# Optimization experiments

Hardware: AMD Instinct MI355X
Metric: run time of the kernel (lower is better)

The kernel has to match this reference:

```python
import jax, jax.numpy as jnp
import numpy as np

FEAT = 1024
SUPPORT = 512
N = 4096


def setup_inputs() -> dict:
    key = jax.random.key(0)
    k1, k2, k3, k4, k5, k6 = jax.random.split(key, 6)
    s = 1.0 / np.sqrt(FEAT)
    f = jax.random.normal(k1, (N, FEAT), dtype=jnp.float32)
    G = jax.random.normal(k2, (SUPPORT, FEAT), dtype=jnp.float32)
    # PyTorch LSTMCell params: weight_ih [4*hidden, input], weight_hh [4*hidden, hidden]
    W_ih = jax.random.uniform(k3, (4 * FEAT, 2 * FEAT), minval=-s, maxval=s, dtype=jnp.float32)
    W_hh = jax.random.uniform(k4, (4 * FEAT, FEAT), minval=-s, maxval=s, dtype=jnp.float32)
    b_ih = jax.random.uniform(k5, (4 * FEAT,), minval=-s, maxval=s, dtype=jnp.float32)
    b_hh = jax.random.uniform(k6, (4 * FEAT,), minval=-s, maxval=s, dtype=jnp.float32)
    return {"f": f, "G": G, "W_ih": W_ih, "W_hh": W_hh, "b_ih": b_ih, "b_hh": b_hh, "n_ways": 20}


def _lstm_cell(x, h, c, W_ih, W_hh, b_ih, b_hh):
    # gates ordered i, f, g, o as in torch.nn.LSTMCell
    gates = x @ W_ih.T + b_ih + h @ W_hh.T + b_hh  # [N, 4*FEAT]
    i, fg, g, o = jnp.split(gates, 4, axis=1)
    i = jax.nn.sigmoid(i)
    fg = jax.nn.sigmoid(fg)
    g = jnp.tanh(g)
    o = jax.nn.sigmoid(o)
    c_new = fg * c + i * g
    h_new = o * jnp.tanh(c_new)
    return h_new, c_new


def reference(f, G, W_ih, W_hh, b_ih, b_hh, n_ways):
    h = f
    c = jnp.zeros_like(f)  # c_0 expanded, zeros (non-learned Variable)
    for _ in range(n_ways):
        logit_a = h @ G.T                      # [N, M]
        a = jax.nn.softmax(logit_a, axis=0)    # softmax over dim 0, as in original
        r = a @ G                              # [N, FEAT]
        x = jnp.concatenate((f, r), axis=1)    # [N, 2*FEAT]
        h, c = _lstm_cell(x, h, c, W_ih, W_hh, b_ih, b_hh)
        h = h + f
    return h
```

## Files before the change

### kernel.cpp

```cpp
#include <hip/hip_runtime.h>
#include <math.h>

#define NB    4096
#define FEAT  1024
#define MSUP  512
#define G4    4096
#define NWAYS 20

typedef _Float16 f16;
typedef f16 f16x8 __attribute__((ext_vector_type(8)));
typedef f16 f16x4 __attribute__((ext_vector_type(4)));
typedef float f32x4 __attribute__((ext_vector_type(4)));
typedef unsigned int u32;
#define GLOBAL_AS __attribute__((address_space(1)))
#define LDS_AS    __attribute__((address_space(3)))

__device__ __forceinline__ void load_lds16(const void* g, void* l) {
    __builtin_amdgcn_global_load_lds((const GLOBAL_AS u32*)g, (LDS_AS u32*)l, 16, 0, 0);
}

__device__ __forceinline__ float sigm(float x) { return 1.f / (1.f + __expf(-x)); }

template<int BM, int BN, int WROWS, int WCOLS, bool OUTF16, bool HASBIAS>
__global__ __launch_bounds__(256) void mfma_nt(
    void* __restrict__ Cv, int ldc,
    const f16* __restrict__ A1, int lda1, const f16* __restrict__ B1, int ldb1, int K1,
    const f16* __restrict__ A2, int lda2, const f16* __restrict__ B2, int ldb2, int K2,
    const f16* __restrict__ A3, int lda3, const f16* __restrict__ B3, int ldb3, int K3,
    const float* __restrict__ bias)
{
    constexpr int BK = 32;
    constexpr int WM = BM / WROWS, WN = BN / WCOLS;
    constexpr int FM = WM / 16,   FN = WN / 16;
    __shared__ f16 As[BM][BK];
    __shared__ f16 Bs[BN][BK];
    const int tid  = threadIdx.x;
    const int lane = tid & 63;
    const int wrow = (tid >> 6) % WROWS, wcol = (tid >> 6) / WROWS;
    const int bm = blockIdx.y * BM, bn = blockIdx.x * BN;
    const int lr = lane & 15, lq = lane >> 4;

    f32x4 acc[FM][FN] = {};

    #pragma unroll
    for (int pass = 0; pass < 3; ++pass) {
        const f16* A = pass == 0 ? A1 : (pass == 1 ? A2 : A3);
        const f16* B = pass == 0 ? B1 : (pass == 1 ? B2 : B3);
        const int lda = pass == 0 ? lda1 : (pass == 1 ? lda2 : lda3);
        const int ldb = pass == 0 ? ldb1 : (pass == 1 ? ldb2 : ldb3);
        const int K   = pass == 0 ? K1  : (pass == 1 ? K2  : K3);
        if (!A) break;
        #pragma unroll 1
        for (int k0 = 0; k0 < K; k0 += BK) {
            __syncthreads();
            #pragma unroll
            for (int t = 0; t < (BM * 4) / 256; ++t) {
                int c = t * 256 + tid;
                load_lds16(A + (size_t)(bm + (c >> 2)) * lda + k0 + (c & 3) * 8,
                           &As[0][0] + ((size_t)t * 256 + (tid & 192)) * 8);
            }
            #pragma unroll
            for (int t = 0; t < (BN * 4) / 256; ++t) {
                int c = t * 256 + tid;
                load_lds16(B + (size_t)(bn + (c >> 2)) * ldb + k0 + (c & 3) * 8,
                           &Bs[0][0] + ((size_t)t * 256 + (tid & 192)) * 8);
            }
            __syncthreads();
            f16x8 af[FM], bf[FN];
            #pragma unroll
            for (int i = 0; i < FM; ++i)
                af[i] = *(const f16x8*)&As[wrow * WM + i * 16 + lr][lq * 8];
            #pragma unroll
            for (int j = 0; j < FN; ++j)
                bf[j] = *(const f16x8*)&Bs[wcol * WN + j * 16 + lr][lq * 8];
            #pragma unroll
            for (int i = 0; i < FM; ++i)
                #pragma unroll
                for (int j = 0; j < FN; ++j)
                    acc[i][j] = __builtin_amdgcn_mfma_f32_16x16x32_f16(af[i], bf[j], acc[i][j], 0, 0, 0);
        }
    }

    #pragma unroll
    for (int i = 0; i < FM; ++i) {
        #pragma unroll
        for (int j = 0; j < FN; ++j) {
            const int col  = bn + wcol * WN + j * 16 + lr;
            const int row0 = bm + wrow * WM + i * 16 + lq * 4;
            float badd = HASBIAS ? bias[col] : 0.f;
            #pragma unroll
            for (int r = 0; r < 4; ++r) {
                size_t off = (size_t)(row0 + r) * ldc + col;
                float v = acc[i][j][r] + badd;
                if (OUTF16) ((f16*)Cv)[off] = (f16)v;
                else        ((float*)Cv)[off] = v;
            }
        }
    }
}

__global__ __launch_bounds__(256) void gates_fused(
    const f16* __restrict__ a,
    const f16* __restrict__ WrHi,
    const f16* __restrict__ WrLo,
    const f16* __restrict__ h,
    const f16* __restrict__ Whh,
    const f16* __restrict__ pre,
    const float* __restrict__ fin,
    float* __restrict__ cbuf,
    f16* __restrict__ hh,
    float* __restrict__ hout,
    int first, int writeH)
{
    constexpr int BM = 128, BN = 128, BK = 32;
    constexpr int WM = 64, WN = 64, FM = 4, FN = 4;
    __shared__ f16 As[BM][BK];
    __shared__ f16 BsH[BN][BK];
    __shared__ f16 BsL[BN][BK];
    const int tid  = threadIdx.x;
    const int lane = tid & 63;
    const int wrow = (tid >> 6) & 1, wcol = (tid >> 6) >> 1;
    const int bm = blockIdx.y * BM, bn = blockIdx.x * BN;
    const int lr = lane & 15, lq = lane >> 4;

    f32x4 acc[FM][FN] = {};

    #pragma unroll 1
    for (int k0 = 0; k0 < MSUP; k0 += BK) {
        __syncthreads();
        #pragma unroll
        for (int t = 0; t < 2; ++t) {
            int c = t * 256 + tid;
            load_lds16(a + (size_t)(bm + (c >> 2)) * MSUP + k0 + (c & 3) * 8,
                       &As[0][0] + ((size_t)t * 256 + (tid & 192)) * 8);
        }
        #pragma unroll
        for (int t = 0; t < 2; ++t) {
            int c = t * 256 + tid;
            load_lds16(WrHi + (size_t)(bn + (c >> 2)) * MSUP + k0 + (c & 3) * 8,
                       &BsH[0][0] + ((size_t)t * 256 + (tid & 192)) * 8);
        }
        #pragma unroll
        for (int t = 0; t < 2; ++t) {
            int c = t * 256 + tid;
            load_lds16(WrLo + (size_t)(bn + (c >> 2)) * MSUP + k0 + (c & 3) * 8,
                       &BsL[0][0] + ((size_t)t * 256 + (tid & 192)) * 8);
        }
        __syncthreads();
        f16x8 af[FM], bh[FN], bl[FN];
        #pragma unroll
        for (int i = 0; i < FM; ++i)
            af[i] = *(const f16x8*)&As[wrow * WM + i * 16 + lr][lq * 8];
        #pragma unroll
        for (int j = 0; j < FN; ++j) {
            bh[j] = *(const f16x8*)&BsH[wcol * WN + j * 16 + lr][lq * 8];
            bl[j] = *(const f16x8*)&BsL[wcol * WN + j * 16 + lr][lq * 8];
        }
        #pragma unroll
        for (int i = 0; i < FM; ++i)
            #pragma unroll
            for (int j = 0; j < FN; ++j) {
                acc[i][j] = __builtin_amdgcn_mfma_f32_16x16x32_f16(af[i], bh[j], acc[i][j], 0, 0, 0);
                acc[i][j] = __builtin_amdgcn_mfma_f32_16x16x32_f16(af[i], bl[j], acc[i][j], 0, 0, 0);
            }
    }

    #pragma unroll 1
    for (int k0 = 0; k0 < FEAT; k0 += BK) {
        __syncthreads();
        #pragma unroll
        for (int t = 0; t < 2; ++t) {
            int c = t * 256 + tid;
            load_lds16(h + (size_t)(bm + (c >> 2)) * FEAT + k0 + (c & 3) * 8,
                       &As[0][0] + ((size_t)t * 256 + (tid & 192)) * 8);
        }
        #pragma unroll
        for (int t = 0; t < 2; ++t) {
            int c = t * 256 + tid;
            load_lds16(Whh + (size_t)(bn + (c >> 2)) * FEAT + k0 + (c & 3) * 8,
                       &BsH[0][0] + ((size_t)t * 256 + (tid & 192)) * 8);
        }
        __syncthreads();
        f16x8 af[FM], bf[FN];
        #pragma unroll
        for (int i = 0; i < FM; ++i)
            af[i] = *(const f16x8*)&As[wrow * WM + i * 16 + lr][lq * 8];
        #pragma unroll
        for (int j = 0; j < FN; ++j)
            bf[j] = *(const f16x8*)&BsH[wcol * WN + j * 16 + lr][lq * 8];
        #pragma unroll
        for (int i = 0; i < FM; ++i)
            #pragma unroll
            for (int j = 0; j < FN; ++j)
                acc[i][j] = __builtin_amdgcn_mfma_f32_16x16x32_f16(af[i], bf[j], acc[i][j], 0, 0, 0);
    }

    const int q  = lane & 3;
    const int kk = (lane >> 2) & 3;
    #pragma unroll
    for (int i = 0; i < FM; ++i) {
        #pragma unroll
        for (int j = 0; j < FN; ++j) {
            const int cb   = bn + wcol * WN + j * 16;
            const int row0 = bm + wrow * WM + i * 16 + lq * 4;
            float x[4];
            #pragma unroll
            for (int r = 0; r < 4; ++r) x[r] = acc[i][j][r];
            float g4[4];
            #pragma unroll
            for (int k = 0; k < 4; ++k) {
                int srcq = (q + k) & 3;
                int src  = (lane & ~3) | srcq;
                g4[srcq] = __shfl(x[(q - k + 4) & 3], src, 64);
            }
            const int row  = row0 + q;
            const int feat = (cb >> 2) + kk;
            f16x4 p = *(const f16x4*)(pre + (size_t)row * G4 + cb + 4 * kk);
            const float i_ = sigm(g4[0] + (float)p[0]);
            const float f_ = sigm(g4[1] + (float)p[1]);
            const float g_ = tanhf(g4[2] + (float)p[2]);
            const float o_ = sigm(g4[3] + (float)p[3]);
            const size_t cid = ((size_t)(blockIdx.y * gridDim.x + blockIdx.x) * (FM * FN)
                                + i * FN + j) * 256 + tid;
            float cold = first ? 0.f : cbuf[cid];
            float cn = i_ * g_ + f_ * cold;
            cbuf[cid] = cn;
            float hn = o_ * tanhf(cn) + fin[(size_t)row * FEAT + feat];
            hh[(size_t)row * FEAT + feat] = (f16)hn;
            if (writeH) hout[(size_t)row * FEAT + feat] = hn;
        }
    }
}

__global__ __launch_bounds__(256) void softmax_rows_kernel(
    const float* __restrict__ X, f16* __restrict__ Y)
{
    const int row = blockIdx.x;
    const float* x = X + (size_t)row * NB;
    f16* y = Y + (size_t)row * NB;
    const int tid = threadIdx.x;
    float v[16];
    float mx = -1e30f;
    #pragma unroll
    for (int i = 0; i < 16; ++i) { v[i] = x[tid + (i << 8)]; mx = fmaxf(mx, v[i]); }
    #pragma unroll
    for (int off = 32; off > 0; off >>= 1) mx = fmaxf(mx, __shfl_down(mx, off));
    __shared__ float sm[4];
    if ((tid & 63) == 0) sm[tid >> 6] = mx;
    __syncthreads();
    mx = fmaxf(fmaxf(sm[0], sm[1]), fmaxf(sm[2], sm[3]));
    float s = 0.f;
    #pragma unroll
    for (int i = 0; i < 16; ++i) { v[i] = __expf(v[i] - mx); s += v[i]; }
    #pragma unroll
    for (int off = 32; off > 0; off >>= 1) s += __shfl_down(s, off);
    __shared__ float ss[4];
    if ((tid & 63) == 0) ss[tid >> 6] = s;
    __syncthreads();
    s = ss[0] + ss[1] + ss[2] + ss[3];
    const float inv = 1.f / s;
    #pragma unroll
    for (int i = 0; i < 16; ++i) y[tid + (i << 8)] = (f16)(v[i] * inv);
}

__global__ __launch_bounds__(256) void transpose_f16_kernel(
    const f16* __restrict__ in, f16* __restrict__ out, int R, int C)
{
    __shared__ f16 t[64][65];
    const int r0 = blockIdx.y * 64, c0 = blockIdx.x * 64;
    const int lr = threadIdx.x & 63, lw = threadIdx.x >> 6;
    #pragma unroll
    for (int i = 0; i < 16; ++i) {
        int rr = lw * 16 + i;
        t[rr][lr] = in[(size_t)(r0 + rr) * C + c0 + lr];
    }
    __syncthreads();
    #pragma unroll
    for (int i = 0; i < 16; ++i) {
        int cc = lw * 16 + i;
        out[(size_t)(c0 + cc) * R + r0 + lr] = t[lr][cc];
    }
}

__global__ __launch_bounds__(256) void cvt_f16_kernel(
    const float* __restrict__ in, f16* __restrict__ out, int n)
{
    int idx = (blockIdx.x * 256 + threadIdx.x) * 4;
    if (idx < n) {
        float4 v = *(const float4*)(in + idx);
        f16x4 o = {(f16)v.x, (f16)v.y, (f16)v.z, (f16)v.w};
        *(f16x4*)(out + idx) = o;
    }
}

__global__ __launch_bounds__(256) void cvt_perm_kernel(
    const float* __restrict__ in, f16* __restrict__ out, int ld)
{
    int idx = (blockIdx.x * 256 + threadIdx.x) * 4;
    int j = idx / ld, k = idx % ld;
    int dst = 4 * (j & 1023) + (j >> 10);
    float4 v = *(const float4*)(in + idx);
    f16x4 o = {(f16)v.x, (f16)v.y, (f16)v.z, (f16)v.w};
    *(f16x4*)(out + (size_t)dst * ld + k) = o;
}

__global__ __launch_bounds__(256) void bias_perm_kernel(
    const float* __restrict__ bih, const float* __restrict__ bhh, float* __restrict__ out)
{
    int j = blockIdx.x * 256 + threadIdx.x;
    out[4 * (j & 1023) + (j >> 10)] = bih[j] + bhh[j];
}

__global__ __launch_bounds__(256) void split_hilo_kernel(
    const float* __restrict__ in, f16* __restrict__ hi, f16* __restrict__ lo, int n)
{
    int idx = (blockIdx.x * 256 + threadIdx.x) * 4;
    if (idx < n) {
        float4 v = *(const float4*)(in + idx);
        f16x4 h = {(f16)v.x, (f16)v.y, (f16)v.z, (f16)v.w};
        f16x4 l = {(f16)(v.x - (float)h.x), (f16)(v.y - (float)h.y),
                   (f16)(v.z - (float)h.z), (f16)(v.w - (float)h.w)};
        *(f16x4*)(hi + idx) = h;
        *(f16x4*)(lo + idx) = l;
    }
}

extern "C" void kernel_launch(void* const* d_in, const int* in_sizes, int n_in,
                              void* d_out, int out_size, void* d_ws, size_t ws_size,
                              hipStream_t stream) {
    const float* f   = (const float*)d_in[0];
    const float* G   = (const float*)d_in[1];
    const float* Wih = (const float*)d_in[2];
    const float* Whh = (const float*)d_in[3];
    const float* bih = (const float*)d_in[4];
    const float* bhh = (const float*)d_in[5];
    float* h = (float*)d_out;

    char* W = (char*)d_ws;
    f16*   pre_h   = (f16*)(W);
    float* aT      = (float*)(W + (size_t)(32 << 20));
    f16*   aTh     = (f16*)(W + (size_t)(40 << 20));
    f16*   a_h     = (f16*)(W + (size_t)(44 << 20));
    float* cbuf    = (float*)(W + (size_t)(48 << 20));
    f16*   h0      = (f16*)(W + (size_t)(64 << 20));
    f16*   hA      = (f16*)(W + (size_t)(72 << 20));
    f16*   hB      = (f16*)(W + (size_t)(80 << 20));
    f16*   Wih_h   = (f16*)(W + (size_t)(88 << 20));
    f16*   Whh_h   = (f16*)(W + (size_t)(104 << 20));
    float* Wr32    = (float*)(W + (size_t)(112 << 20));
    f16*   Wr_hi   = (f16*)(W + (size_t)(120 << 20));
    f16*   Wr_lo   = (f16*)(W + (size_t)(124 << 20));
    f16*   G_h     = (f16*)(W + (size_t)(128 << 20));
    float* bias_p  = (float*)(W + (size_t)(129 << 20));

    const f16* NF = nullptr;
    const dim3 blk(256);

    cvt_f16_kernel<<<(NB * FEAT) / 1024, blk, 0, stream>>>(f, h0, NB * FEAT);
    cvt_perm_kernel<<<(G4 * 2 * FEAT) / 1024, blk, 0, stream>>>(Wih, Wih_h, 2 * FEAT);
    cvt_perm_kernel<<<(G4 * FEAT) / 1024, blk, 0, stream>>>(Whh, Whh_h, FEAT);
    cvt_f16_kernel<<<(MSUP * FEAT) / 1024, blk, 0, stream>>>(G, G_h, MSUP * FEAT);
    bias_perm_kernel<<<G4 / 256, blk, 0, stream>>>(bih, bhh, bias_p);

    mfma_nt<128, 128, 2, 2, true, true><<<dim3(G4 / 128, NB / 128), blk, 0, stream>>>(
        pre_h, G4,
        h0, FEAT, Wih_h, 2 * FEAT, FEAT,
        NF, 0, NF, 0, 0, NF, 0, NF, 0, 0,
        bias_p);

    mfma_nt<128, 128, 2, 2, false, false><<<dim3(MSUP / 128, G4 / 128), blk, 0, stream>>>(
        Wr32, MSUP,
        Wih_h + FEAT, 2 * FEAT, G_h, FEAT, FEAT,
        NF, 0, NF, 0, 0, NF, 0, NF, 0, 0,
        nullptr);
    split_hilo_kernel<<<(G4 * MSUP) / 1024, blk, 0, stream>>>(Wr32, Wr_hi, Wr_lo, G4 * MSUP);

    const f16* hcur = h0;
    for (int it = 0; it < NWAYS; ++it) {
        mfma_nt<64, 64, 2, 2, false, false><<<dim3(NB / 64, MSUP / 64), blk, 0, stream>>>(
            aT, NB,
            G_h, FEAT, hcur, FEAT, FEAT,
            NF, 0, NF, 0, 0, NF, 0, NF, 0, 0,
            nullptr);

        softmax_rows_kernel<<<MSUP, blk, 0, stream>>>(aT, aTh);
        transpose_f16_kernel<<<dim3(NB / 64, MSUP / 64), blk, 0, stream>>>(aTh, a_h, MSUP, NB);

        f16* hnext = (it & 1) ? hB : hA;
        gates_fused<<<dim3(G4 / 128, NB / 128), blk, 0, stream>>>(
            a_h, Wr_hi, Wr_lo, hcur, Whh_h,
            pre_h, f, cbuf, hnext, h, it == 0, it == NWAYS - 1);
        hcur = hnext;
    }
}
```

Before: 2.856 ms.

## Rewrite gates GEMM as 256x256 double-buffered 8-wave kernel over concatenated weights

Replaces the 128x128 gates kernel with a 256x256-tile, 512-thread kernel. It uses dynamic LDS double buffering with XOR swizzling, staged async global-to-LDS loads interleaved with the MFMA phases, and s_setprio around the math. The hi/lo Wr halves and W_hh are packed into one concatenated K=2048 weight matrix, so a single K loop covers all three products. Bigger tiles and overlapped loads are meant to raise arithmetic intensity and hide memory latency. The costs are higher register and LDS pressure (128KB dynamic LDS) and a grid of only 256 blocks.

```diff
diff --git a/kernel.cpp b/kernel.cpp
--- a/kernel.cpp
+++ b/kernel.cpp
@@ -99,12 +99,10 @@
     }
 }
 
-__global__ __launch_bounds__(256) void gates_fused(
+__global__ __launch_bounds__(512, 2) void gates_8p(
     const f16* __restrict__ a,
-    const f16* __restrict__ WrHi,
-    const f16* __restrict__ WrLo,
     const f16* __restrict__ h,
-    const f16* __restrict__ Whh,
+    const f16* __restrict__ Wcat,
     const f16* __restrict__ pre,
     const float* __restrict__ fin,
     float* __restrict__ cbuf,
@@ -112,97 +110,144 @@
     float* __restrict__ hout,
     int first, int writeH)
 {
-    constexpr int BM = 128, BN = 128, BK = 32;
-    constexpr int WM = 64, WN = 64, FM = 4, FN = 4;
-    __shared__ f16 As[BM][BK];
-    __shared__ f16 BsH[BN][BK];
-    __shared__ f16 BsL[BN][BK];
+    extern __shared__ f16x8 smem8[];
+    f16* smem = (f16*)smem8;
     const int tid  = threadIdx.x;
     const int lane = tid & 63;
-    const int wrow = (tid >> 6) & 1, wcol = (tid >> 6) >> 1;
-    const int bm = blockIdx.y * BM, bn = blockIdx.x * BN;
+    const int wid  = tid >> 6;
+    const int wrow = wid >> 2, wcol = wid & 3;
     const int lr = lane & 15, lq = lane >> 4;
 
-    f32x4 acc[FM][FN] = {};
+    const int bidr = blockIdx.y * 16 + blockIdx.x;
+    const int wg   = (bidr & 7) * 32 + (bidr >> 3);
+    const int bm = (wg >> 4) * 256;
+    const int bn = (wg & 15) * 256;
+
+    f32x4 acc[8][4] = {};
+
+    auto stage = [&](const f16* src, int ld, int rb, int ko, f16* lbase, int l) {
+        int c = l * 512 + tid;
+        int r = c >> 3;
+        int x = (c & 7) ^ (r & 7);
+        load_lds16(src + (size_t)(rb + r) * ld + ko + (x << 3),
+                   lbase + ((size_t)(l * 512 + (tid & 448))) * 8);
+    };
+    #define RDF(BUF, RB, KK) \
+        (*(const f16x8*)((BUF) + ((size_t)((RB) + lr) << 6) + ((((KK) << 2 | lq) ^ (lr & 7)) << 3)))
+
+    #pragma unroll
+    for (int l = 0; l < 4; ++l) {
+        stage(a,    MSUP, bm, 0, smem,         l);
+        stage(Wcat, 2048, bn, 0, smem + 16384, l);
+    }
 
     #pragma unroll 1
-    for (int k0 = 0; k0 < MSUP; k0 += BK) {
-        __syncthreads();
-        #pragma unroll
-        for (int t = 0; t < 2; ++t) {
-            int c = t * 256 + tid;
-            load_lds16(a + (size_t)(bm + (c >> 2)) * MSUP + k0 + (c & 3) * 8,
-                       &As[0][0] + ((size_t)t * 256 + (tid & 192)) * 8);
+    for (int t = 0; t < 32; ++t) {
+        f16* Ab = smem + (t & 1) * 32768;
+        f16* Bb = Ab + 16384;
+        f16* An = smem + ((t + 1) & 1) * 32768;
+        f16* Bn = An + 16384;
+        const int k1 = (t + 1) * 64;
+        const f16* As2 = a; int lda2 = MSUP, ko2 = k1;
+        if (k1 >= 1024)     { As2 = h; lda2 = FEAT; ko2 = k1 - 1024; }
+        else if (k1 >= 512) { ko2 = k1 - 512; }
+        const bool st = (t < 31);
+
+        f16x8 af[4][2], bf[2][2], bg[2][2];
+
+        if (st) {
+            stage(As2, lda2, bm, ko2, An, 0);
+            stage(Wcat, 2048, bn, k1, Bn, 0);
+            asm volatile("s_waitcnt vmcnt(2)" ::: "memory");
+        } else {
+            asm volatile("s_waitcnt vmcnt(0)" ::: "memory");
         }
-        #pragma unroll
-        for (int t = 0; t < 2; ++t) {
-            int c = t * 256 + tid;
-            load_lds16(WrHi + (size_t)(bn + (c >> 2)) * MSUP + k0 + (c & 3) * 8,
-                       &BsH[0][0] + ((size_t)t * 256 + (tid & 192)) * 8);
-        }
-        #pragma unroll
-        for (int t = 0; t < 2; ++t) {
-            int c = t * 256 + tid;
-            load_lds16(WrLo + (size_t)(bn + (c >> 2)) * MSUP + k0 + (c & 3) * 8,
-                       &BsL[0][0] + ((size_t)t * 256 + (tid & 192)) * 8);
-        }
-        __syncthreads();
-        f16x8 af[FM], bh[FN], bl[FN];
-        #pragma unroll
-        for (int i = 0; i < FM; ++i)
-            af[i] = *(const f16x8*)&As[wrow * WM + i * 16 + lr][lq * 8];
-        #pragma unroll
-        for (int j = 0; j < FN; ++j) {
-            bh[j] = *(const f16x8*)&BsH[wcol * WN + j * 16 + lr][lq * 8];
-            bl[j] = *(const f16x8*)&BsL[wcol * WN + j * 16 + lr][lq * 8];
-        }
-        #pragma unroll
-        for (int i = 0; i < FM; ++i)
-            #pragma unroll
-            for (int j = 0; j < FN; ++j) {
-                acc[i][j] = __builtin_amdgcn_mfma_f32_16x16x32_f16(af[i], bh[j], acc[i][j], 0, 0, 0);
-                acc[i][j] = __builtin_amdgcn_mfma_f32_16x16x32_f16(af[i], bl[j], acc[i][j], 0, 0, 0);
-            }
-    }
-
-    #pragma unroll 1
-    for (int k0 = 0; k0 < FEAT; k0 += BK) {
-        __syncthreads();
-        #pragma unroll
-        for (int t = 0; t < 2; ++t) {
-            int c = t * 256 + tid;
-            load_lds16(h + (size_t)(bm + (c >> 2)) * FEAT + k0 + (c & 3) * 8,
-                       &As[0][0] + ((size_t)t * 256 + (tid & 192)) * 8);
-        }
-        #pragma unroll
-        for (int t = 0; t < 2; ++t) {
-            int c = t * 256 + tid;
-            load_lds16(Whh + (size_t)(bn + (c >> 2)) * FEAT + k0 + (c & 3) * 8,
-                       &BsH[0][0] + ((size_t)t * 256 + (tid & 192)) * 8);
-        }
-        __syncthreads();
-        f16x8 af[FM], bf[FN];
-        #pragma unroll
-        for (int i = 0; i < FM; ++i)
-            af[i] = *(const f16x8*)&As[wrow * WM + i * 16 + lr][lq * 8];
-        #pragma unroll
-        for (int j = 0; j < FN; ++j)
-            bf[j] = *(const f16x8*)&BsH[wcol * WN + j * 16 + lr][lq * 8];
-        #pragma unroll
-        for (int i = 0; i < FM; ++i)
-            #pragma unroll
-            for (int j = 0; j < FN; ++j)
-                acc[i][j] = __builtin_amdgcn_mfma_f32_16x16x32_f16(af[i], bf[j], acc[i][j], 0, 0, 0);
-    }
+        asm volatile("s_barrier" ::: "memory");
+        #pragma unroll
+        for (int i = 0; i < 4; ++i)
+            #pragma unroll
+            for (int kk = 0; kk < 2; ++kk)
+                af[i][kk] = RDF(Ab, wrow * 128 + i * 16, kk);
+        #pragma unroll
+        for (int j = 0; j < 2; ++j)
+            #pragma unroll
+            for (int kk = 0; kk < 2; ++kk)
+                bf[j][kk] = RDF(Bb, wcol * 64 + j * 16, kk);
+        __builtin_amdgcn_s_setprio(1);
+        #pragma unroll
+        for (int kk = 0; kk < 2; ++kk)
+            #pragma unroll
+            for (int i = 0; i < 4; ++i)
+                #pragma unroll
+                for (int j = 0; j < 2; ++j)
+                    acc[i][j] = __builtin_amdgcn_mfma_f32_16x16x32_f16(af[i][kk], bf[j][kk], acc[i][j], 0, 0, 0);
+        __builtin_amdgcn_s_setprio(0);
+        __builtin_amdgcn_s_barrier();
+
+        if (st) { stage(As2, lda2, bm, ko2, An, 1); stage(Wcat, 2048, bn, k1, Bn, 1); }
+        #pragma unroll
+        for (int j = 0; j < 2; ++j)
+            #pragma unroll
+            for (int kk = 0; kk < 2; ++kk)
+                bg[j][kk] = RDF(Bb, wcol * 64 + (j + 2) * 16, kk);
+        __builtin_amdgcn_s_barrier();
+        __builtin_amdgcn_s_setprio(1);
+        #pragma unroll
+        for (int kk = 0; kk < 2; ++kk)
+            #pragma unroll
+            for (int i = 0; i < 4; ++i)
+                #pragma unroll
+                for (int j = 0; j < 2; ++j)
+                    acc[i][j + 2] = __builtin_amdgcn_mfma_f32_16x16x32_f16(af[i][kk], bg[j][kk], acc[i][j + 2], 0, 0, 0);
+        __builtin_amdgcn_s_setprio(0);
+        __builtin_amdgcn_s_barrier();
+
+        if (st) { stage(As2, lda2, bm, ko2, An, 2); stage(Wcat, 2048, bn, k1, Bn, 2); }
+        #pragma unroll
+        for (int i = 0; i < 4; ++i)
+            #pragma unroll
+            for (int kk = 0; kk < 2; ++kk)
+                af[i][kk] = RDF(Ab, wrow * 128 + (i + 4) * 16, kk);
+        __builtin_amdgcn_s_barrier();
+        __builtin_amdgcn_s_setprio(1);
+        #pragma unroll
+        for (int kk = 0; kk < 2; ++kk)
+            #pragma unroll
+            for (int i = 0; i < 4; ++i)
+                #pragma unroll
+                for (int j = 0; j < 2; ++j)
+                    acc[i + 4][j + 2] = __builtin_amdgcn_mfma_f32_16x16x32_f16(af[i][kk], bg[j][kk], acc[i + 4][j + 2], 0, 0, 0);
+        __builtin_amdgcn_s_setprio(0);
+        __builtin_amdgcn_s_barrier();
+
+        if (st) { stage(As2, lda2, bm, ko2, An, 3); stage(Wcat, 2048, bn, k1, Bn, 3); }
+        #pragma unroll
+        for (int j = 0; j < 2; ++j)
+            #pragma unroll
+            for (int kk = 0; kk < 2; ++kk)
+                bf[j][kk] = RDF(Bb, wcol * 64 + j * 16, kk);
+        __builtin_amdgcn_s_barrier();
+        __builtin_amdgcn_s_setprio(1);
+        #pragma unroll
+        for (int kk = 0; kk < 2; ++kk)
+            #pragma unroll
+            for (int i = 0; i < 4; ++i)
+                #pragma unroll
+                for (int j = 0; j < 2; ++j)
+                    acc[i + 4][j] = __builtin_amdgcn_mfma_f32_16x16x32_f16(af[i][kk], bf[j][kk], acc[i + 4][j], 0, 0, 0);
+        __builtin_amdgcn_s_setprio(0);
+        asm volatile("s_barrier" ::: "memory");
+    }
+    #undef RDF
 
     const int q  = lane & 3;
-    const int kk = (lane >> 2) & 3;
-    #pragma unroll
-    for (int i = 0; i < FM; ++i) {
-        #pragma unroll
-        for (int j = 0; j < FN; ++j) {
-            const int cb   = bn + wcol * WN + j * 16;
-            const int row0 = bm + wrow * WM + i * 16 + lq * 4;
+    const int fk = (lane >> 2) & 3;
+    #pragma unroll
+    for (int i = 0; i < 8; ++i) {
+        #pragma unroll
+        for (int j = 0; j < 4; ++j) {
+            const int cb   = bn + wcol * 64 + j * 16;
+            const int row0 = bm + wrow * 128 + i * 16 + lq * 4;
             float x[4];
             #pragma unroll
             for (int r = 0; r < 4; ++r) x[r] = acc[i][j][r];
@@ -214,14 +259,14 @@
                 g4[srcq] = __shfl(x[(q - k + 4) & 3], src, 64);
             }
             const int row  = row0 + q;
-            const int feat = (cb >> 2) + kk;
-            f16x4 p = *(const f16x4*)(pre + (size_t)row * G4 + cb + 4 * kk);
+            const int feat = (cb >> 2) + fk;
+            f16x4 p = *(const f16x4*)(pre + (size_t)row * G4 + cb + 4 * fk);
             const float i_ = sigm(g4[0] + (float)p[0]);
             const float f_ = sigm(g4[1] + (float)p[1]);
             const float g_ = tanhf(g4[2] + (float)p[2]);
             const float o_ = sigm(g4[3] + (float)p[3]);
-            const size_t cid = ((size_t)(blockIdx.y * gridDim.x + blockIdx.x) * (FM * FN)
-                                + i * FN + j) * 256 + tid;
+            const size_t cid = ((size_t)(blockIdx.y * gridDim.x + blockIdx.x) * 32
+                                + i * 4 + j) * 512 + tid;
             float cold = first ? 0.f : cbuf[cid];
             float cn = i_ * g_ + f_ * cold;
             cbuf[cid] = cn;
@@ -294,14 +339,14 @@
 }
 
 __global__ __launch_bounds__(256) void cvt_perm_kernel(
-    const float* __restrict__ in, f16* __restrict__ out, int ld)
+    const float* __restrict__ in, f16* __restrict__ out, int ld_in, int ld_out, int col_off)
 {
     int idx = (blockIdx.x * 256 + threadIdx.x) * 4;
-    int j = idx / ld, k = idx % ld;
+    int j = idx / ld_in, k = idx % ld_in;
     int dst = 4 * (j & 1023) + (j >> 10);
     float4 v = *(const float4*)(in + idx);
     f16x4 o = {(f16)v.x, (f16)v.y, (f16)v.z, (f16)v.w};
-    *(f16x4*)(out + (size_t)dst * ld + k) = o;
+    *(f16x4*)(out + (size_t)dst * ld_out + col_off + k) = o;
 }
 
 __global__ __launch_bounds__(256) void bias_perm_kernel(
@@ -311,18 +356,17 @@
     out[4 * (j & 1023) + (j >> 10)] = bih[j] + bhh[j];
 }
 
-__global__ __launch_bounds__(256) void split_hilo_kernel(
-    const float* __restrict__ in, f16* __restrict__ hi, f16* __restrict__ lo, int n)
+__global__ __launch_bounds__(256) void split_wcat_kernel(
+    const float* __restrict__ in, f16* __restrict__ out)
 {
     int idx = (blockIdx.x * 256 + threadIdx.x) * 4;
-    if (idx < n) {
-        float4 v = *(const float4*)(in + idx);
-        f16x4 h = {(f16)v.x, (f16)v.y, (f16)v.z, (f16)v.w};
-        f16x4 l = {(f16)(v.x - (float)h.x), (f16)(v.y - (float)h.y),
-                   (f16)(v.z - (float)h.z), (f16)(v.w - (float)h.w)};
-        *(f16x4*)(hi + idx) = h;
-        *(f16x4*)(lo + idx) = l;
-    }
+    int g = idx >> 9, k = idx & 511;
+    float4 v = *(const float4*)(in + idx);
+    f16x4 hi = {(f16)v.x, (f16)v.y, (f16)v.z, (f16)v.w};
+    f16x4 lo = {(f16)(v.x - (float)hi.x), (f16)(v.y - (float)hi.y),
+                (f16)(v.z - (float)hi.z), (f16)(v.w - (float)hi.w)};
+    *(f16x4*)(out + (size_t)g * 2048 + k) = hi;
+    *(f16x4*)(out + (size_t)g * 2048 + 512 + k) = lo;
 }
 
 extern "C" void kernel_launch(void* const* d_in, const int* in_sizes, int n_in,
@@ -346,19 +390,20 @@
     f16*   hA      = (f16*)(W + (size_t)(72 << 20));
     f16*   hB      = (f16*)(W + (size_t)(80 << 20));
     f16*   Wih_h   = (f16*)(W + (size_t)(88 << 20));
-    f16*   Whh_h   = (f16*)(W + (size_t)(104 << 20));
-    float* Wr32    = (float*)(W + (size_t)(112 << 20));
-    f16*   Wr_hi   = (f16*)(W + (size_t)(120 << 20));
-    f16*   Wr_lo   = (f16*)(W + (size_t)(124 << 20));
+    f16*   Wcat    = (f16*)(W + (size_t)(104 << 20));
+    float* Wr32    = (float*)(W + (size_t)(120 << 20));
     f16*   G_h     = (f16*)(W + (size_t)(128 << 20));
     float* bias_p  = (float*)(W + (size_t)(129 << 20));
 
     const f16* NF = nullptr;
     const dim3 blk(256);
 
+    hipFuncSetAttribute((const void*)gates_8p,
+                        hipFuncAttributeMaxDynamicSharedMemorySize, 131072);
+
     cvt_f16_kernel<<<(NB * FEAT) / 1024, blk, 0, stream>>>(f, h0, NB * FEAT);
-    cvt_perm_kernel<<<(G4 * 2 * FEAT) / 1024, blk, 0, stream>>>(Wih, Wih_h, 2 * FEAT);
-    cvt_perm_kernel<<<(G4 * FEAT) / 1024, blk, 0, stream>>>(Whh, Whh_h, FEAT);
+    cvt_perm_kernel<<<(G4 * 2 * FEAT) / 1024, blk, 0, stream>>>(Wih, Wih_h, 2 * FEAT, 2 * FEAT, 0);
+    cvt_perm_kernel<<<(G4 * FEAT) / 1024, blk, 0, stream>>>(Whh, Wcat, FEAT, 2048, 1024);
     cvt_f16_kernel<<<(MSUP * FEAT) / 1024, blk, 0, stream>>>(G, G_h, MSUP * FEAT);
     bias_perm_kernel<<<G4 / 256, blk, 0, stream>>>(bih, bhh, bias_p);
 
@@ -373,7 +418,7 @@
         Wih_h + FEAT, 2 * FEAT, G_h, FEAT, FEAT,
         NF, 0, NF, 0, 0, NF, 0, NF, 0, 0,
         nullptr);
-    split_hilo_kernel<<<(G4 * MSUP) / 1024, blk, 0, stream>>>(Wr32, Wr_hi, Wr_lo, G4 * MSUP);
+    split_wcat_kernel<<<(G4 * MSUP) / 1024, blk, 0, stream>>>(Wr32, Wcat);
 
     const f16* hcur = h0;
     for (int it = 0; it < NWAYS; ++it) {
@@ -387,9 +432,8 @@
         transpose_f16_kernel<<<dim3(NB / 64, MSUP / 64), blk, 0, stream>>>(aTh, a_h, MSUP, NB);
 
         f16* hnext = (it & 1) ? hB : hA;
-        gates_fused<<<dim3(G4 / 128, NB / 128), blk, 0, stream>>>(
-            a_h, Wr_hi, Wr_lo, hcur, Whh_h,
-            pre_h, f, cbuf, hnext, h, it == 0, it == NWAYS - 1);
+        gates_8p<<<dim3(G4 / 256, NB / 256), 512, 131072, stream>>>(
+            a_h, hcur, Wcat, pre_h, f, cbuf, hnext, h, it == 0, it == NWAYS - 1);
         hcur = hnext;
     }
 }
```

After: 2.435 ms. 1.17x faster.
